# Optimization experiments

Hardware: AMD Instinct MI355X
Metric: run time of the kernel (lower is better)

The kernel has to match this reference:

```python
import jax, jax.numpy as jnp
import numpy as np

B, N, D, K = 16, 512, 256, 12  # batch, nodes, node_dim, num edge types (4 arg + 4 arg' + punct +/- + no_edges +/-)
ITERATION_STEPS = 1


def setup_inputs() -> dict:
    key = jax.random.key(0)
    ks = jax.random.split(key, 8)
    node = jax.random.normal(ks[0], (B, N, D), dtype=jnp.float32)
    node_mask = jax.random.randint(ks[1], (B, N), 0, 2, dtype=jnp.int32)
    graphs = jax.random.randint(ks[2], (K, B, N, N), 0, 2, dtype=jnp.int32)
    s = 1.0 / np.sqrt(D)
    Ww = jax.random.normal(ks[3], (1, D), dtype=jnp.float32) * s   # _node_weight_fc
    bw = jnp.zeros((1,), dtype=jnp.float32)
    Ws = jax.random.normal(ks[4], (D, D), dtype=jnp.float32) * s   # _self_node_fc
    bs = jnp.zeros((D,), dtype=jnp.float32)
    Wk = jax.random.normal(ks[5], (K, D, D), dtype=jnp.float32) * s  # 12 bias-free per-edge-type linears
    return {"node": node, "Ww": Ww, "bw": bw, "Ws": Ws, "bs": bs, "Wk": Wk,
            "node_mask": node_mask, "graphs": graphs}


def reference(node, Ww, bw, Ws, bs, Wk, node_mask, graphs):
    dt = node.dtype
    mask = node_mask.astype(dt)
    eye = jnp.eye(N, dtype=dt)
    # dd_graph = mask_row * mask_col * (1 - diag)
    dd = mask[:, None, :] * mask[:, :, None] * (1.0 - eye)          # [B,N,N]
    g = dd[None] * graphs.astype(dt)                                # [K,B,N,N] masked adjacencies
    neigh = g.sum(axis=(0, 3))                                      # [B,N] total neighbor count
    neigh = jnp.where(neigh >= 1, neigh, jnp.ones((), dt))

    all_w = []
    for _ in range(ITERATION_STEPS):
        # (1) node relatedness
        w = jax.nn.sigmoid(node @ Ww.T + bw)[..., 0]                # [B,N]
        all_w.append(w)
        self_info = node @ Ws.T + bs                                # [B,N,D]
        # (2) message propagation for all 12 edge types, batched
        trans = jnp.einsum('bnd,ked->kbne', node, Wk)               # [K,B,N,D] per-type linear (x @ W.T)
        wg = w[None, :, None, :] * g                                # [K,B,N,N] masked node weights
        agg = jnp.einsum('kbmn,kbnd->bmd', wg, trans) / neigh[..., None]
        # (3) update
        node = jax.nn.relu(self_info + agg)

    all_weight = jnp.stack(all_w, axis=1)                           # [B,steps,N]
    return node, all_weight
```

## Files before the change

### kernel.cpp

```cpp
#include <hip/hip_runtime.h>
#include <hip/hip_bf16.h>
#include <math.h>

#define BB 16
#define NN 512
#define DD 256
#define KK 12

typedef __bf16 bf16x8 __attribute__((ext_vector_type(8)));
typedef __bf16 bf16x4 __attribute__((ext_vector_type(4)));
typedef float  f32x4  __attribute__((ext_vector_type(4)));

#define WS_WM     0
#define WS_MASKBF 32768
#define WS_NODEBF 49152
#define WS_NODET  4243456
#define WS_WKBF   8437760
#define WS_WSBF   10010624

#define BAR() do { \
    __builtin_amdgcn_sched_barrier(0); \
    asm volatile("s_waitcnt lgkmcnt(0)" ::: "memory"); \
    __builtin_amdgcn_s_barrier(); \
    __builtin_amdgcn_sched_barrier(0); \
} while (0)

__global__ __launch_bounds__(256) void k1_prep(const float* __restrict__ node,
        const float* __restrict__ Ww, const float* __restrict__ bw,
        const int* __restrict__ node_mask,
        float* __restrict__ wm, __bf16* __restrict__ maskbf,
        __bf16* __restrict__ node_bf, float* __restrict__ all_w) {
    int t = threadIdx.x;
    int lane = t & 63;
    int row = blockIdx.x * 4 + (t >> 6);
    const float4 nv = *(const float4*)(node + (size_t)row * DD + lane * 4);
    const float4 wv = *(const float4*)(Ww + lane * 4);
    float dot = nv.x*wv.x + nv.y*wv.y + nv.z*wv.z + nv.w*wv.w;
    #pragma unroll
    for (int off = 32; off > 0; off >>= 1) dot += __shfl_xor(dot, off);
    float w = 1.0f / (1.0f + expf(-(dot + bw[0])));
    int mk = node_mask[row];
    if (lane == 0) {
        wm[row]     = w * (float)mk;
        all_w[row]  = w;
        maskbf[row] = (__bf16)(float)mk;
    }
    bf16x4 nb = {(__bf16)nv.x, (__bf16)nv.y, (__bf16)nv.z, (__bf16)nv.w};
    *(bf16x4*)(node_bf + (size_t)row * DD + lane * 4) = nb;
}

__global__ __launch_bounds__(256) void k1b_convert(const float* __restrict__ Wk,
        const float* __restrict__ Ws, __bf16* __restrict__ Wk_bf, __bf16* __restrict__ Ws_bf) {
    const int KDD = KK * DD * DD;
    int idx = (blockIdx.x * 256 + threadIdx.x) * 4;
    if (idx < KDD) {
        float4 v = *(const float4*)(Wk + idx);
        bf16x4 o = {(__bf16)v.x, (__bf16)v.y, (__bf16)v.z, (__bf16)v.w};
        *(bf16x4*)(Wk_bf + idx) = o;
    } else {
        int j = idx - KDD;
        if (j < DD * DD) {
            float4 v = *(const float4*)(Ws + j);
            bf16x4 o = {(__bf16)v.x, (__bf16)v.y, (__bf16)v.z, (__bf16)v.w};
            *(bf16x4*)(Ws_bf + j) = o;
        }
    }
}

__global__ __launch_bounds__(256) void k2_transpose(const float* __restrict__ node,
        const float* __restrict__ wm, __bf16* __restrict__ dst) {
    __shared__ float tile[64][65];
    int bx = blockIdx.x;
    int b = bx >> 5; int rest = bx & 31; int nt = rest >> 2; int dt = rest & 3;
    int n0 = nt * 64, d0 = dt * 64;
    int t = threadIdx.x;
    #pragma unroll
    for (int i = 0; i < 16; i++) {
        int idx = i * 256 + t;
        int n = idx >> 6, d = idx & 63;
        tile[n][d] = node[((size_t)(b * NN + n0 + n)) * DD + d0 + d];
    }
    __syncthreads();
    #pragma unroll
    for (int i = 0; i < 16; i++) {
        int idx = i * 256 + t;
        int d = idx >> 6, n = idx & 63;
        float w = wm[b * NN + n0 + n];
        dst[((size_t)(b * DD + d0 + d)) * NN + n0 + n] = (__bf16)(tile[n][d] * w);
    }
}

__global__ __launch_bounds__(512, 2) void k45_fused(const int* __restrict__ graphs,
        const int* __restrict__ node_mask, const __bf16* __restrict__ maskbf,
        const __bf16* __restrict__ node_t, const __bf16* __restrict__ node_bf,
        const __bf16* __restrict__ Wk_bf, const __bf16* __restrict__ Ws_bf,
        const float* __restrict__ bs, float* __restrict__ out) {
    __shared__ __align__(16) __bf16 Abf[32][520];
    __shared__ __align__(16) __bf16 Tk[2][32][264];
    __shared__ float cntp[8][32];
    __shared__ float sm[32];
    int bx = blockIdx.x;
    int xcd  = bx & 7;
    int dh   = (bx >> 3) & 1;
    int pair = bx >> 4;
    int tile = xcd * 32 + pair;
    int b  = tile >> 4;
    int mt = tile & 15;
    int m0 = mt * 32;
    int d0 = dh * 128;
    int t = threadIdx.x;
    int lane = t & 63;
    int w = t >> 6;
    int q = lane >> 4;
    int l16 = lane & 15;
    int esub = w * 32;
    int dsub = d0 + w * 16;

    int crow = t >> 7;
    int ccol = (t & 127) * 4;

    f32x4 accO[2];
    accO[0] = (f32x4){0.f, 0.f, 0.f, 0.f};
    accO[1] = (f32x4){0.f, 0.f, 0.f, 0.f};
    f32x4 accC[2];
    accC[0] = (f32x4){0.f, 0.f, 0.f, 0.f};
    accC[1] = (f32x4){0.f, 0.f, 0.f, 0.f};

    int4 g[8];

#define LOADG(kk_) do { \
        const int4* gb = (const int4*)(graphs + ((size_t)(((kk_) * BB + b) * NN + m0)) * NN); \
        _Pragma("unroll") \
        for (int u = 0; u < 8; u++) g[u] = gb[u * 512 + t]; \
    } while (0)

#define CONVERT() do { \
        _Pragma("unroll") \
        for (int u = 0; u < 8; u++) { \
            int row = u * 4 + crow; \
            unsigned p0 = (unsigned)g[u].x | ((unsigned)g[u].y << 16); \
            unsigned p1 = (unsigned)g[u].z | ((unsigned)g[u].w << 16); \
            unsigned drel = (unsigned)(m0 + row - ccol); \
            if (drel < 2u)      p0 &= ~(0xFFFFu << (16 * drel)); \
            else if (drel < 4u) p1 &= ~(0xFFFFu << (16 * (drel - 2))); \
            uint2 st; st.x = p0 * 0x3F80u; st.y = p1 * 0x3F80u; \
            *(uint2*)&Abf[row][ccol] = st; \
        } \
    } while (0)

    LOADG(0);
    CONVERT();
    LOADG(1);
    BAR();

    int tc = 0;

    #pragma unroll 1
    for (int k = 0; k < KK; k++) {
        f32x4 accT[2][2];
        #pragma unroll
        for (int i = 0; i < 2; i++)
            #pragma unroll
            for (int jj = 0; jj < 2; jj++) accT[i][jj] = (f32x4){0.f, 0.f, 0.f, 0.f};
        #pragma unroll
        for (int kk = 0; kk < 16; kk++) {
            int n0c = kk * 32;
            bf16x8 af[2], bfr[2];
            #pragma unroll
            for (int fm = 0; fm < 2; fm++)
                af[fm] = *(const bf16x8*)&Abf[fm * 16 + l16][n0c + q * 8];
            #pragma unroll
            for (int fd = 0; fd < 2; fd++)
                bfr[fd] = *(const bf16x8*)(node_t +
                    ((size_t)(b * DD + esub + fd * 16 + l16)) * NN + n0c + q * 8);
            #pragma unroll
            for (int fm = 0; fm < 2; fm++)
                #pragma unroll
                for (int fd = 0; fd < 2; fd++)
                    accT[fm][fd] = __builtin_amdgcn_mfma_f32_16x16x32_bf16(
                        af[fm], bfr[fd], accT[fm][fd], 0, 0, 0);
            if ((kk >> 1) == w) {
                bf16x8 bfm = (bf16x8){0,0,0,0,0,0,0,0};
                if (l16 == 0)
                    bfm = *(const bf16x8*)(maskbf + b * NN + n0c + q * 8);
                accC[0] = __builtin_amdgcn_mfma_f32_16x16x32_bf16(af[0], bfm, accC[0], 0, 0, 0);
                accC[1] = __builtin_amdgcn_mfma_f32_16x16x32_bf16(af[1], bfm, accC[1], 0, 0, 0);
            }
        }

        #pragma unroll
        for (int fm = 0; fm < 2; fm++)
            #pragma unroll
            for (int fd = 0; fd < 2; fd++) {
                int col = esub + fd * 16 + l16;
                #pragma unroll
                for (int r = 0; r < 4; r++)
                    Tk[tc][fm * 16 + q * 4 + r][col] = (__bf16)accT[fm][fd][r];
            }

        BAR();

        if (k < KK - 1) CONVERT();
        if (k < KK - 2) LOADG(k + 2);

        #pragma unroll
        for (int ee = 0; ee < 8; ee++) {
            int e0c = ee * 32;
            bf16x8 afT[2];
            #pragma unroll
            for (int fm = 0; fm < 2; fm++)
                afT[fm] = *(const bf16x8*)&Tk[tc][fm * 16 + l16][e0c + q * 8];
            bf16x8 bw2 = *(const bf16x8*)(Wk_bf +
                ((size_t)(k * DD + dsub + l16)) * DD + e0c + q * 8);
            #pragma unroll
            for (int fm = 0; fm < 2; fm++)
                accO[fm] = __builtin_amdgcn_mfma_f32_16x16x32_bf16(
                    afT[fm], bw2, accO[fm], 0, 0, 0);
        }

        BAR();
        tc ^= 1;
    }

    if (l16 == 0) {
        #pragma unroll
        for (int fm = 0; fm < 2; fm++)
            #pragma unroll
            for (int r = 0; r < 4; r++)
                cntp[w][fm * 16 + q * 4 + r] = accC[fm][r];
    }
    __syncthreads();
    if (t < 32) {
        float c = 0.0f;
        #pragma unroll
        for (int w8 = 0; w8 < 8; w8++) c += cntp[w8][t];
        int mk = node_mask[b * NN + m0 + t];
        sm[t] = (float)mk / (c >= 0.5f ? c : 1.0f);
    }
    __syncthreads();

    #pragma unroll
    for (int fm = 0; fm < 2; fm++)
        #pragma unroll
        for (int r = 0; r < 4; r++)
            accO[fm][r] *= sm[fm * 16 + q * 4 + r];

    #pragma unroll
    for (int ee = 0; ee < 8; ee++) {
        int e0c = ee * 32;
        bf16x8 afS[2];
        #pragma unroll
        for (int fm = 0; fm < 2; fm++)
            afS[fm] = *(const bf16x8*)(node_bf +
                ((size_t)(b * NN + m0 + fm * 16 + l16)) * DD + e0c + q * 8);
        bf16x8 bwS = *(const bf16x8*)(Ws_bf +
            ((size_t)(dsub + l16)) * DD + e0c + q * 8);
        #pragma unroll
        for (int fm = 0; fm < 2; fm++)
            accO[fm] = __builtin_amdgcn_mfma_f32_16x16x32_bf16(
                afS[fm], bwS, accO[fm], 0, 0, 0);
    }

    {
        int d = dsub + l16;
        float bsv = bs[d];
        #pragma unroll
        for (int fm = 0; fm < 2; fm++)
            #pragma unroll
            for (int r = 0; r < 4; r++) {
                int m = m0 + fm * 16 + q * 4 + r;
                float v = accO[fm][r] + bsv;
                out[((size_t)(b * NN + m)) * DD + d] = fmaxf(v, 0.0f);
            }
    }
#undef LOADG
#undef CONVERT
}

extern "C" void kernel_launch(void* const* d_in, const int* in_sizes, int n_in,
                              void* d_out, int out_size, void* d_ws, size_t ws_size,
                              hipStream_t stream) {
    const float* node      = (const float*)d_in[0];
    const float* Ww        = (const float*)d_in[1];
    const float* bw        = (const float*)d_in[2];
    const float* Ws        = (const float*)d_in[3];
    const float* bs        = (const float*)d_in[4];
    const float* Wk        = (const float*)d_in[5];
    const int*   node_mask = (const int*)d_in[6];
    const int*   graphs    = (const int*)d_in[7];
    float* out   = (float*)d_out;
    float* all_w = out + (size_t)BB * NN * DD;

    char* ws = (char*)d_ws;
    float*  wm      = (float*)(ws + WS_WM);
    __bf16* maskbf  = (__bf16*)(ws + WS_MASKBF);
    __bf16* node_bf = (__bf16*)(ws + WS_NODEBF);
    __bf16* node_t  = (__bf16*)(ws + WS_NODET);
    __bf16* Wk_bf   = (__bf16*)(ws + WS_WKBF);
    __bf16* Ws_bf   = (__bf16*)(ws + WS_WSBF);

    k1_prep    <<<2048, 256, 0, stream>>>(node, Ww, bw, node_mask, wm, maskbf, node_bf, all_w);
    k1b_convert<<< 832, 256, 0, stream>>>(Wk, Ws, Wk_bf, Ws_bf);
    k2_transpose<<<512, 256, 0, stream>>>(node, wm, node_t);
    k45_fused  <<< 512, 512, 0, stream>>>(graphs, node_mask, maskbf, node_t, node_bf,
                                          Wk_bf, Ws_bf, bs, out);
}
```

Before: 391.4 us.

## Use 1024-thread blocks covering full D and double-buffer adjacency tile

The fused aggregation kernel now launches 256 blocks of 1024 threads, each covering all 256 output features for a 32-row tile. Before, two 512-thread blocks split D in half and each re-read and re-converted the same graph tile. The adjacency LDS buffer is double-buffered, so the next edge type's conversion can happen before the barrier and one barrier per iteration is dropped. This halves the redundant graph traffic and synchronisation, but gives one block per CU with fewer waves per SIMD, and removes the XCD-aware tile mapping.

Result: no change. 391.1 us (-0.1%).

```diff
diff --git a/kernel.cpp b/kernel.cpp
--- a/kernel.cpp
+++ b/kernel.cpp
@@ -90,31 +90,26 @@
     }
 }
 
-__global__ __launch_bounds__(512, 2) void k45_fused(const int* __restrict__ graphs,
+__global__ __launch_bounds__(1024, 1) void k45_fused(const int* __restrict__ graphs,
         const int* __restrict__ node_mask, const __bf16* __restrict__ maskbf,
         const __bf16* __restrict__ node_t, const __bf16* __restrict__ node_bf,
         const __bf16* __restrict__ Wk_bf, const __bf16* __restrict__ Ws_bf,
         const float* __restrict__ bs, float* __restrict__ out) {
-    __shared__ __align__(16) __bf16 Abf[32][520];
+    __shared__ __align__(16) __bf16 Abf[2][32][520];
     __shared__ __align__(16) __bf16 Tk[2][32][264];
-    __shared__ float cntp[8][32];
+    __shared__ float cntp[16][32];
     __shared__ float sm[32];
     int bx = blockIdx.x;
-    int xcd  = bx & 7;
-    int dh   = (bx >> 3) & 1;
-    int pair = bx >> 4;
-    int tile = xcd * 32 + pair;
-    int b  = tile >> 4;
-    int mt = tile & 15;
+    int b  = (bx & 7) + 8 * ((bx >> 3) & 1);
+    int mt = bx >> 4;
     int m0 = mt * 32;
-    int d0 = dh * 128;
     int t = threadIdx.x;
     int lane = t & 63;
     int w = t >> 6;
     int q = lane >> 4;
     int l16 = lane & 15;
-    int esub = w * 32;
-    int dsub = d0 + w * 16;
+    int esub = w * 16;
+    int dsub = w * 16;
 
     int crow = t >> 7;
     int ccol = (t & 127) * 4;
@@ -126,60 +121,54 @@
     accC[0] = (f32x4){0.f, 0.f, 0.f, 0.f};
     accC[1] = (f32x4){0.f, 0.f, 0.f, 0.f};
 
-    int4 g[8];
+    int4 g[4];
 
 #define LOADG(kk_) do { \
         const int4* gb = (const int4*)(graphs + ((size_t)(((kk_) * BB + b) * NN + m0)) * NN); \
         _Pragma("unroll") \
-        for (int u = 0; u < 8; u++) g[u] = gb[u * 512 + t]; \
+        for (int u = 0; u < 4; u++) g[u] = gb[u * 1024 + t]; \
     } while (0)
 
-#define CONVERT() do { \
+#define CONVERT(nb_) do { \
         _Pragma("unroll") \
-        for (int u = 0; u < 8; u++) { \
-            int row = u * 4 + crow; \
+        for (int u = 0; u < 4; u++) { \
+            int row = u * 8 + crow; \
             unsigned p0 = (unsigned)g[u].x | ((unsigned)g[u].y << 16); \
             unsigned p1 = (unsigned)g[u].z | ((unsigned)g[u].w << 16); \
             unsigned drel = (unsigned)(m0 + row - ccol); \
             if (drel < 2u)      p0 &= ~(0xFFFFu << (16 * drel)); \
             else if (drel < 4u) p1 &= ~(0xFFFFu << (16 * (drel - 2))); \
             uint2 st; st.x = p0 * 0x3F80u; st.y = p1 * 0x3F80u; \
-            *(uint2*)&Abf[row][ccol] = st; \
+            *(uint2*)&Abf[nb_][row][ccol] = st; \
         } \
     } while (0)
 
     LOADG(0);
-    CONVERT();
+    CONVERT(0);
     LOADG(1);
     BAR();
 
-    int tc = 0;
+    int ac = 0, tc = 0;
 
     #pragma unroll 1
     for (int k = 0; k < KK; k++) {
-        f32x4 accT[2][2];
-        #pragma unroll
-        for (int i = 0; i < 2; i++)
-            #pragma unroll
-            for (int jj = 0; jj < 2; jj++) accT[i][jj] = (f32x4){0.f, 0.f, 0.f, 0.f};
+        f32x4 accT[2];
+        accT[0] = (f32x4){0.f, 0.f, 0.f, 0.f};
+        accT[1] = (f32x4){0.f, 0.f, 0.f, 0.f};
         #pragma unroll
         for (int kk = 0; kk < 16; kk++) {
             int n0c = kk * 32;
-            bf16x8 af[2], bfr[2];
-            #pragma unroll
-            for (int fm = 0; fm < 2; fm++)
-                af[fm] = *(const bf16x8*)&Abf[fm * 16 + l16][n0c + q * 8];
-            #pragma unroll
-            for (int fd = 0; fd < 2; fd++)
-                bfr[fd] = *(const bf16x8*)(node_t +
-                    ((size_t)(b * DD + esub + fd * 16 + l16)) * NN + n0c + q * 8);
-            #pragma unroll
-            for (int fm = 0; fm < 2; fm++)
-                #pragma unroll
-                for (int fd = 0; fd < 2; fd++)
-                    accT[fm][fd] = __builtin_amdgcn_mfma_f32_16x16x32_bf16(
-                        af[fm], bfr[fd], accT[fm][fd], 0, 0, 0);
-            if ((kk >> 1) == w) {
+            bf16x8 af[2];
+            #pragma unroll
+            for (int fm = 0; fm < 2; fm++)
+                af[fm] = *(const bf16x8*)&Abf[ac][fm * 16 + l16][n0c + q * 8];
+            bf16x8 bfr = *(const bf16x8*)(node_t +
+                ((size_t)(b * DD + esub + l16)) * NN + n0c + q * 8);
+            #pragma unroll
+            for (int fm = 0; fm < 2; fm++)
+                accT[fm] = __builtin_amdgcn_mfma_f32_16x16x32_bf16(
+                    af[fm], bfr, accT[fm], 0, 0, 0);
+            if (kk == w) {
                 bf16x8 bfm = (bf16x8){0,0,0,0,0,0,0,0};
                 if (l16 == 0)
                     bfm = *(const bf16x8*)(maskbf + b * NN + n0c + q * 8);
@@ -188,20 +177,19 @@
             }
         }
 
-        #pragma unroll
-        for (int fm = 0; fm < 2; fm++)
-            #pragma unroll
-            for (int fd = 0; fd < 2; fd++) {
-                int col = esub + fd * 16 + l16;
+        if (k < KK - 1) CONVERT(ac ^ 1);
+        if (k < KK - 2) LOADG(k + 2);
+
+        {
+            int col = esub + l16;
+            #pragma unroll
+            for (int fm = 0; fm < 2; fm++)
                 #pragma unroll
                 for (int r = 0; r < 4; r++)
-                    Tk[tc][fm * 16 + q * 4 + r][col] = (__bf16)accT[fm][fd][r];
-            }
+                    Tk[tc][fm * 16 + q * 4 + r][col] = (__bf16)accT[fm][r];
+        }
 
         BAR();
-
-        if (k < KK - 1) CONVERT();
-        if (k < KK - 2) LOADG(k + 2);
 
         #pragma unroll
         for (int ee = 0; ee < 8; ee++) {
@@ -218,8 +206,7 @@
                     afT[fm], bw2, accO[fm], 0, 0, 0);
         }
 
-        BAR();
-        tc ^= 1;
+        ac ^= 1; tc ^= 1;
     }
 
     if (l16 == 0) {
@@ -233,7 +220,7 @@
     if (t < 32) {
         float c = 0.0f;
         #pragma unroll
-        for (int w8 = 0; w8 < 8; w8++) c += cntp[w8][t];
+        for (int w16 = 0; w16 < 16; w16++) c += cntp[w16][t];
         int mk = node_mask[b * NN + m0 + t];
         sm[t] = (float)mk / (c >= 0.5f ? c : 1.0f);
     }
@@ -302,6 +289,6 @@
     k1_prep    <<<2048, 256, 0, stream>>>(node, Ww, bw, node_mask, wm, maskbf, node_bf, all_w);
     k1b_convert<<< 832, 256, 0, stream>>>(Wk, Ws, Wk_bf, Ws_bf);
     k2_transpose<<<512, 256, 0, stream>>>(node, wm, node_t);
-    k45_fused  <<< 512, 512, 0, stream>>>(graphs, node_mask, maskbf, node_t, node_bf,
-                                          Wk_bf, Ws_bf, bs, out);
-}
+    k45_fused  <<< 256, 1024, 0, stream>>>(graphs, node_mask, maskbf, node_t, node_bf,
+                                           Wk_bf, Ws_bf, bs, out);
+}
```
